# Kernel optimization log

Measured on AMD Instinct MI355X. Metric: run time of the kernel, lower is better.

The kernel has to match this reference:

```python
import jax, jax.numpy as jnp
import numpy as np

# FCHL19 hyperparameters (from init_kwargs defaults)
NSPEC = 4
RCUT = 6.0
NRS2 = 24
NRS3 = 20
ETA2 = 0.32
ETA3 = 2.7
TWO_BODY_DECAY = 1.8
THREE_BODY_WEIGHT = float(np.sqrt(2.7 / np.pi) * 13.4)  # sqrt(eta3/pi)*13.4, as in __init__
THREE_BODY_DECAY = 0.57
PI = float(np.pi)
NPAIRS = NSPEC * (NSPEC + 1) // 2  # 10 unordered element pairs
RS2 = jnp.linspace(0.0, RCUT, NRS2 + 1)[1:]
RS3 = jnp.linspace(0.0, RCUT, NRS3 + 1)[1:]


def setup_inputs() -> dict:
    key = jax.random.key(0)
    k1, k2, k3 = jax.random.split(key, 3)
    B, A = 64, 48
    X = jax.random.uniform(k1, (B, A, 3), jnp.float32, 0.0, 12.0)  # coords in 12 A box
    Z = jax.random.randint(k2, (B, A), 0, NSPEC, dtype=jnp.int32)  # species indices into [1,6,7,8]
    atom_counts = jax.random.randint(k3, (B,), 24, A + 1, dtype=jnp.int32)
    atomIDs = (jnp.arange(B * A, dtype=jnp.int32) % A)
    molIDs = (jnp.arange(B * A, dtype=jnp.int32) // A)
    return {"X": X, "Z": Z, "atomIDs": atomIDs, "molIDs": molIDs, "atom_counts": atom_counts}


def _fchl_rep(X, Z, atom_counts):
    B, A, _ = X.shape
    idx = jnp.arange(A)
    valid = idx[None, :] < atom_counts[:, None]                       # [B,A]
    diff = X[:, :, None, :] - X[:, None, :, :]                        # [B,A,A,3] (X_i - X_j)
    r2 = jnp.sum(diff * diff, axis=-1)
    eye = jnp.eye(A, dtype=bool)
    pmask = valid[:, :, None] & valid[:, None, :] & ~eye              # [B,A,A]
    r = jnp.sqrt(jnp.where(pmask, r2, 1.0))
    within = pmask & (r < RCUT)
    rs = jnp.where(within, r, 1.0)                                    # safe distances
    fc = jnp.where(within, 0.5 * (jnp.cos(PI * rs / RCUT) + 1.0), 0.0)

    # ---- two-body: log-normal radial basis with power-law scaling ----
    s2 = jnp.log1p(ETA2 / (rs * rs))                                  # sigma^2
    mu = jnp.log(rs) - 0.5 * s2
    pref = fc / (rs ** TWO_BODY_DECAY) / (jnp.sqrt(s2) * np.sqrt(2.0 * PI))
    radial2 = (pref[..., None] / RS2) * jnp.exp(
        -(jnp.log(RS2) - mu[..., None]) ** 2 / (2.0 * s2[..., None]))  # [B,A,A,nRs2]
    eoh = jax.nn.one_hot(Z, NSPEC, dtype=X.dtype) * valid[..., None]  # [B,A,S]
    rep2 = jnp.einsum('bijk,bjs->bisk', radial2, eoh).reshape(B, A, NSPEC * NRS2)

    # ---- three-body: ATM-weighted radial x (cos,sin) angular, pairs k>j ----
    rij = rs[:, :, :, None]   # [B,A(i),A(j),1]
    rik = rs[:, :, None, :]   # [B,A(i),1,A(k)]
    rjk = rs[:, None, :, :]   # [B,1,A(j),A(k)]
    cos_i = jnp.einsum('bijx,bikx->bijk', diff, diff) / (rij * rik)
    cos_i = jnp.clip(cos_i, -1.0, 1.0)
    cos_j = (rij * rij + rjk * rjk - rik * rik) / (2.0 * rij * rjk)
    cos_k = (rik * rik + rjk * rjk - rij * rij) / (2.0 * rik * rjk)
    mask3 = (within[:, :, :, None] & within[:, :, None, :]
             & (idx[None, :] > idx[:, None])[None, None, :, :])        # k > j
    ksi3 = THREE_BODY_WEIGHT * (1.0 + 3.0 * cos_i * cos_j * cos_k) \
        / (rij * rik * rjk) ** THREE_BODY_DECAY
    w = jnp.where(mask3, ksi3 * fc[:, :, :, None] * fc[:, :, None, :], 0.0)
    wc = w * cos_i
    ws = w * jnp.sqrt(jnp.clip(1.0 - cos_i * cos_i, 0.0, 1.0))
    d = 0.5 * (rij + rik)                                             # [B,A,A,A]

    # unordered element-pair bin for (Z_j, Z_k)
    ej = Z[:, :, None]
    ek = Z[:, None, :]
    pmin = jnp.minimum(ej, ek)
    pmax = jnp.maximum(ej, ek)
    pidx = pmin * (2 * NSPEC - pmin - 1) // 2 + pmax                  # [B,A,A]
    poh = jax.nn.one_hot(pidx, NPAIRS, dtype=X.dtype)                 # [B,A,A,P]

    def step(carry, Rl):
        rad = jnp.exp(-ETA3 * (d - Rl) ** 2)
        rc = jnp.einsum('bijk,bjkp->bip', wc * rad, poh)
        rsn = jnp.einsum('bijk,bjkp->bip', ws * rad, poh)
        return carry, jnp.stack([rc, rsn], axis=-1)                   # [B,A,P,2]

    _, rep3 = jax.lax.scan(step, 0, RS3)                              # [nRs3,B,A,P,2]
    rep3 = jnp.transpose(rep3, (1, 2, 3, 0, 4)).reshape(B, A, NPAIRS * NRS3 * 2)
    return jnp.concatenate([rep2, rep3], axis=-1)                     # [B,A,496]


def reference(X, Z, atomIDs, molIDs, atom_counts):
    # atomIDs/molIDs are CUDA work-distribution lists; math-irrelevant here.
    return _fchl_rep(X, Z, atom_counts)
```

## Files before the change

kernel.cpp:

```cpp
#include <hip/hip_runtime.h>
#include <math.h>

#define B_MOL 64
#define A_MAX 48
#define NSPEC 4
#define NRS2 24
#define NRS3 20
#define NPAIRS 10
#define REP2 (NSPEC * NRS2)
#define REP3 (NPAIRS * NRS3 * 2)
#define REPTOT (REP2 + REP3)
#define TRIP_CAP 1084

#define RCUT_F 6.0f
#define ETA2_F 0.32f
#define ETA3_F 2.7f
#define PI_F 3.14159265358979323846f
#define W3_F 12.4225780586f
#define SQRT_2PI_F 2.5066282746310002f

__device__ __forceinline__ void decode_tri(int t, int m, int& a_out, int& c_out) {
    const float fm = (float)(2 * m - 1);
    const float disc = fm * fm - 8.0f * (float)t;
    const float sq = __builtin_amdgcn_sqrtf(disc);
    int a = (int)((fm - sq) * 0.5f);
    if (a < 0) a = 0;
    while (a > 0 && (a * (2 * m - 1 - a)) / 2 > t) --a;
    while (((a + 1) * (2 * m - 1 - (a + 1))) / 2 <= t) ++a;
    a_out = a;
    c_out = t - (a * (2 * m - 1 - a)) / 2 + a + 1;
}

__global__ __launch_bounds__(256, 8) void fchl_kernel(
    const float* __restrict__ X, const int* __restrict__ Z,
    const int* __restrict__ atom_counts, float* __restrict__ out)
{
    __shared__ float nb_dx[A_MAX], nb_dy[A_MAX], nb_dz[A_MAX];
    __shared__ float nb_r[A_MAX], nb_r2[A_MAX], nb_rinv[A_MAX];
    __shared__ float nb_fc[A_MAX], nb_mu[A_MAX], nb_i2s2[A_MAX], nb_pref[A_MAX];
    __shared__ int   nb_z[A_MAX], nb_si[A_MAX];
    __shared__ float trip_wc[TRIP_CAP], trip_ws[TRIP_CAP], trip_d[TRIP_CAP];
    __shared__ int   cnt_s[NSPEC];
    __shared__ int   nb_m;

    const int bi = blockIdx.x;
    const int b = bi / A_MAX;
    const int i = bi % A_MAX;
    const int tid = threadIdx.x;
    const int cnt = atom_counts[b];
    float* orow = out + (size_t)bi * REPTOT;

    if (i >= cnt) {
        for (int t = tid; t < REPTOT; t += 256) orow[t] = 0.0f;
        return;
    }

    if (tid < 64) {
        const float xi = X[(b * A_MAX + i) * 3 + 0];
        const float yi = X[(b * A_MAX + i) * 3 + 1];
        const float zi = X[(b * A_MAX + i) * 3 + 2];

        bool flag = false;
        float dx = 0.f, dy = 0.f, dz = 0.f, r = 1.f;
        int zj = 0;
        if (tid < A_MAX && tid < cnt) {
            dx = xi - X[(b * A_MAX + tid) * 3 + 0];
            dy = yi - X[(b * A_MAX + tid) * 3 + 1];
            dz = zi - X[(b * A_MAX + tid) * 3 + 2];
            zj = Z[b * A_MAX + tid];
            r = __builtin_amdgcn_sqrtf(dx * dx + dy * dy + dz * dz);
            flag = (tid != i) && (r < RCUT_F);
        }
        const unsigned long long ms0 = __ballot(flag && zj == 0);
        const unsigned long long ms1 = __ballot(flag && zj == 1);
        const unsigned long long ms2 = __ballot(flag && zj == 2);
        const unsigned long long ms3 = __ballot(flag && zj == 3);
        const unsigned long long mask = ms0 | ms1 | ms2 | ms3;
        if (flag) {
            const unsigned long long below = (1ull << tid) - 1ull;
            const int pos = __popcll(mask & below);
            nb_dx[pos] = dx; nb_dy[pos] = dy; nb_dz[pos] = dz;
            nb_r[pos]  = r;  nb_r2[pos] = r * r;
            nb_rinv[pos] = __builtin_amdgcn_rcpf(r);
            nb_z[pos]  = zj;
            const unsigned long long msp = (zj == 0) ? ms0 : (zj == 1) ? ms1
                                         : (zj == 2) ? ms2 : ms3;
            nb_si[pos] = __popcll(msp & below);
            const float fc = 0.5f * (__cosf(PI_F * r * (1.0f / RCUT_F)) + 1.0f);
            const float lr = __logf(r);
            const float s2 = log1pf(ETA2_F / (r * r));
            nb_fc[pos]   = fc;
            nb_mu[pos]   = lr - 0.5f * s2;
            nb_i2s2[pos] = 0.5f * __builtin_amdgcn_rcpf(s2);
            nb_pref[pos] = fc * __expf(-1.8f * lr) *
                           __builtin_amdgcn_rcpf(__builtin_amdgcn_sqrtf(s2) * SQRT_2PI_F);
        }
        if (tid == 0) {
            cnt_s[0] = (int)__popcll(ms0);
            cnt_s[1] = (int)__popcll(ms1);
            cnt_s[2] = (int)__popcll(ms2);
            cnt_s[3] = (int)__popcll(ms3);
            nb_m = (int)__popcll(mask);
        }
    }
    __syncthreads();

    const int m  = nb_m;
    const int c0 = cnt_s[0], c1 = cnt_s[1], c2 = cnt_s[2], c3 = cnt_s[3];
    const int S0 = (c0 * (c0 - 1)) >> 1;
    const int S1 = c0 * c1, S2 = c0 * c2, S3 = c0 * c3;
    const int S4 = (c1 * (c1 - 1)) >> 1;
    const int S5 = c1 * c2, S6 = c1 * c3;
    const int S7 = (c2 * (c2 - 1)) >> 1;
    const int S8 = c2 * c3;
    const int ntrip = m * (m - 1) / 2;

    for (int t = tid; t < ntrip; t += 256) {
        int a, c;
        decode_tri(t, m, a, c);

        const float rij = nb_r[a], rik = nb_r[c];
        const float r2ij = nb_r2[a], r2ik = nb_r2[c];
        const float rinv_a = nb_rinv[a], rinv_c = nb_rinv[c];
        const float djx = nb_dx[a], djy = nb_dy[a], djz = nb_dz[a];
        const float dkx = nb_dx[c], dky = nb_dy[c], dkz = nb_dz[c];

        float cosi = (djx * dkx + djy * dky + djz * dkz) * rinv_a * rinv_c;
        cosi = fminf(1.0f, fmaxf(-1.0f, cosi));

        const float ex = dkx - djx, ey = dky - djy, ez = dkz - djz;
        const float rjk2 = ex * ex + ey * ey + ez * ez;
        const float rjk = __builtin_amdgcn_sqrtf(rjk2);
        const bool w_jk = (rjk < RCUT_F);
        const float rjke  = w_jk ? rjk : 1.0f;
        const float rjke2 = w_jk ? rjk2 : 1.0f;
        const float rinv_jk = w_jk ? __builtin_amdgcn_rcpf(rjk) : 1.0f;

        const float cosj = (r2ij + rjke2 - r2ik) * 0.5f * rinv_a * rinv_jk;
        const float cosk = (r2ik + rjke2 - r2ij) * 0.5f * rinv_c * rinv_jk;

        const float ksi = W3_F * (1.0f + 3.0f * cosi * cosj * cosk)
                        * __expf(-0.57f * __logf(rij * rik * rjke));
        const float w  = ksi * nb_fc[a] * nb_fc[c];
        const float s1v = fmaxf(1.0f - cosi * cosi, 0.0f);

        const int za = nb_z[a], zc = nb_z[c];
        const int ia = nb_si[a], ic = nb_si[c];
        const int pmn = min(za, zc), pmx = max(za, zc);
        const int p = (pmn * (2 * NSPEC - pmn - 1)) / 2 + pmx;
        int rank;
        if (za == zc) {
            const int cs = (za == 0) ? c0 : (za == 1) ? c1 : (za == 2) ? c2 : c3;
            rank = ia * cs - ((ia * (ia + 1)) >> 1) + (ic - ia - 1);
        } else {
            const int cmx = (pmx == 0) ? c0 : (pmx == 1) ? c1 : (pmx == 2) ? c2 : c3;
            const int iu = (za < zc) ? ia : ic;
            const int iv = (za < zc) ? ic : ia;
            rank = iu * cmx + iv;
        }
        int slot = rank;
        slot += (p > 0) ? S0 : 0;  slot += (p > 1) ? S1 : 0;
        slot += (p > 2) ? S2 : 0;  slot += (p > 3) ? S3 : 0;
        slot += (p > 4) ? S4 : 0;  slot += (p > 5) ? S5 : 0;
        slot += (p > 6) ? S6 : 0;  slot += (p > 7) ? S7 : 0;
        slot += (p > 8) ? S8 : 0;

        trip_wc[slot] = w * cosi;
        trip_ws[slot] = w * __builtin_amdgcn_sqrtf(s1v);
        trip_d[slot]  = 0.5f * (rij + rik);
    }
    __syncthreads();

    if (tid < NPAIRS * NRS3) {
        const int p = tid / NRS3;
        const int l = tid % NRS3;
        const float Rl = 0.3f * (float)(l + 1);
        int s0 = 0;
        s0 += (p > 0) ? S0 : 0;  s0 += (p > 1) ? S1 : 0;
        s0 += (p > 2) ? S2 : 0;  s0 += (p > 3) ? S3 : 0;
        s0 += (p > 4) ? S4 : 0;  s0 += (p > 5) ? S5 : 0;
        s0 += (p > 6) ? S6 : 0;  s0 += (p > 7) ? S7 : 0;
        s0 += (p > 8) ? S8 : 0;
        const int sz = (p == 0) ? S0 : (p == 1) ? S1 : (p == 2) ? S2
                     : (p == 3) ? S3 : (p == 4) ? S4 : (p == 5) ? S5
                     : (p == 6) ? S6 : (p == 7) ? S7 : (p == 8) ? S8
                     : (ntrip - s0);
        const int s1 = s0 + sz;

        float ac0 = 0.0f, as0 = 0.0f, ac1 = 0.0f, as1 = 0.0f;
        int s = s0;
        for (; s + 1 < s1; s += 2) {
            const float d0 = trip_d[s],     d1 = trip_d[s + 1];
            const float dd0 = d0 - Rl,      dd1 = d1 - Rl;
            const float e0 = __expf(-ETA3_F * dd0 * dd0);
            const float e1 = __expf(-ETA3_F * dd1 * dd1);
            ac0 += trip_wc[s] * e0;     as0 += trip_ws[s] * e0;
            ac1 += trip_wc[s + 1] * e1; as1 += trip_ws[s + 1] * e1;
        }
        if (s < s1) {
            const float dd = trip_d[s] - Rl;
            const float e = __expf(-ETA3_F * dd * dd);
            ac0 += trip_wc[s] * e;  as0 += trip_ws[s] * e;
        }
        orow[REP2 + p * (NRS3 * 2) + l * 2 + 0] = ac0 + ac1;
        orow[REP2 + p * (NRS3 * 2) + l * 2 + 1] = as0 + as1;
    } else {
        for (int t2 = tid - 200; t2 < REP2; t2 += 56) {
            const int sp = t2 / NRS2;
            const int n = t2 % NRS2;
            const float Rn = 0.25f * (float)(n + 1);
            const float logRn = __logf(Rn);
            float acc = 0.0f;
            for (int a = 0; a < m; ++a) {
                if (nb_z[a] == sp) {
                    const float dmu = logRn - nb_mu[a];
                    acc += nb_pref[a] * __expf(-dmu * dmu * nb_i2s2[a]);
                }
            }
            orow[t2] = acc * __builtin_amdgcn_rcpf(Rn);
        }
    }
}

extern "C" void kernel_launch(void* const* d_in, const int* in_sizes, int n_in,
                              void* d_out, int out_size, void* d_ws, size_t ws_size,
                              hipStream_t stream) {
    const float* X           = (const float*)d_in[0];
    const int*   Z           = (const int*)d_in[1];
    const int*   atom_counts = (const int*)d_in[4];
    float* out = (float*)d_out;

    fchl_kernel<<<B_MOL * A_MAX, 256, 0, stream>>>(X, Z, atom_counts, out);
}
```

Before: 73.57 us.

## Build neighbor list per wave and overlap two-body with triplet phase

Every wave now builds the neighbor list redundantly, using wave-level ballots and only a wave barrier. This removes the block-wide barrier between neighbor setup and triplet generation. The two-body radial terms move to the last wave and run at the same time as triplet generation on the first three waves. A per-species sorted neighbor index lets the two-body loop skip the species test. Triplet data is packed into one float4 array for single LDS loads. The trade-offs are redundant work across waves and benign same-value LDS write races, and triplet generation now uses 192 threads instead of 256.

```diff
diff --git a/kernel.cpp b/kernel.cpp
--- a/kernel.cpp
+++ b/kernel.cpp
@@ -38,15 +38,14 @@
     __shared__ float nb_dx[A_MAX], nb_dy[A_MAX], nb_dz[A_MAX];
     __shared__ float nb_r[A_MAX], nb_r2[A_MAX], nb_rinv[A_MAX];
     __shared__ float nb_fc[A_MAX], nb_mu[A_MAX], nb_i2s2[A_MAX], nb_pref[A_MAX];
-    __shared__ int   nb_z[A_MAX], nb_si[A_MAX];
-    __shared__ float trip_wc[TRIP_CAP], trip_ws[TRIP_CAP], trip_d[TRIP_CAP];
-    __shared__ int   cnt_s[NSPEC];
-    __shared__ int   nb_m;
+    __shared__ int   nb_z[A_MAX], nb_si[A_MAX], snb[A_MAX];
+    __shared__ float4 trip4[TRIP_CAP];
 
     const int bi = blockIdx.x;
     const int b = bi / A_MAX;
     const int i = bi % A_MAX;
     const int tid = threadIdx.x;
+    const int lane = tid & 63;
     const int cnt = atom_counts[b];
     float* orow = out + (size_t)bi * REPTOT;
 
@@ -55,58 +54,55 @@
         return;
     }
 
-    if (tid < 64) {
-        const float xi = X[(b * A_MAX + i) * 3 + 0];
-        const float yi = X[(b * A_MAX + i) * 3 + 1];
-        const float zi = X[(b * A_MAX + i) * 3 + 2];
-
-        bool flag = false;
-        float dx = 0.f, dy = 0.f, dz = 0.f, r = 1.f;
-        int zj = 0;
-        if (tid < A_MAX && tid < cnt) {
-            dx = xi - X[(b * A_MAX + tid) * 3 + 0];
-            dy = yi - X[(b * A_MAX + tid) * 3 + 1];
-            dz = zi - X[(b * A_MAX + tid) * 3 + 2];
-            zj = Z[b * A_MAX + tid];
-            r = __builtin_amdgcn_sqrtf(dx * dx + dy * dy + dz * dz);
-            flag = (tid != i) && (r < RCUT_F);
-        }
-        const unsigned long long ms0 = __ballot(flag && zj == 0);
-        const unsigned long long ms1 = __ballot(flag && zj == 1);
-        const unsigned long long ms2 = __ballot(flag && zj == 2);
-        const unsigned long long ms3 = __ballot(flag && zj == 3);
-        const unsigned long long mask = ms0 | ms1 | ms2 | ms3;
-        if (flag) {
-            const unsigned long long below = (1ull << tid) - 1ull;
-            const int pos = __popcll(mask & below);
-            nb_dx[pos] = dx; nb_dy[pos] = dy; nb_dz[pos] = dz;
-            nb_r[pos]  = r;  nb_r2[pos] = r * r;
-            nb_rinv[pos] = __builtin_amdgcn_rcpf(r);
-            nb_z[pos]  = zj;
-            const unsigned long long msp = (zj == 0) ? ms0 : (zj == 1) ? ms1
-                                         : (zj == 2) ? ms2 : ms3;
-            nb_si[pos] = __popcll(msp & below);
-            const float fc = 0.5f * (__cosf(PI_F * r * (1.0f / RCUT_F)) + 1.0f);
-            const float lr = __logf(r);
-            const float s2 = log1pf(ETA2_F / (r * r));
-            nb_fc[pos]   = fc;
-            nb_mu[pos]   = lr - 0.5f * s2;
-            nb_i2s2[pos] = 0.5f * __builtin_amdgcn_rcpf(s2);
-            nb_pref[pos] = fc * __expf(-1.8f * lr) *
-                           __builtin_amdgcn_rcpf(__builtin_amdgcn_sqrtf(s2) * SQRT_2PI_F);
-        }
-        if (tid == 0) {
-            cnt_s[0] = (int)__popcll(ms0);
-            cnt_s[1] = (int)__popcll(ms1);
-            cnt_s[2] = (int)__popcll(ms2);
-            cnt_s[3] = (int)__popcll(ms3);
-            nb_m = (int)__popcll(mask);
-        }
-    }
-    __syncthreads();
-
-    const int m  = nb_m;
-    const int c0 = cnt_s[0], c1 = cnt_s[1], c2 = cnt_s[2], c3 = cnt_s[3];
+    const float xi = X[(b * A_MAX + i) * 3 + 0];
+    const float yi = X[(b * A_MAX + i) * 3 + 1];
+    const float zi = X[(b * A_MAX + i) * 3 + 2];
+
+    bool flag = false;
+    float dx = 0.f, dy = 0.f, dz = 0.f, r = 1.f;
+    int zj = 0;
+    if (lane < A_MAX && lane < cnt) {
+        dx = xi - X[(b * A_MAX + lane) * 3 + 0];
+        dy = yi - X[(b * A_MAX + lane) * 3 + 1];
+        dz = zi - X[(b * A_MAX + lane) * 3 + 2];
+        zj = Z[b * A_MAX + lane];
+        r = __builtin_amdgcn_sqrtf(dx * dx + dy * dy + dz * dz);
+        flag = (lane != i) && (r < RCUT_F);
+    }
+    const unsigned long long ms0 = __ballot(flag && zj == 0);
+    const unsigned long long ms1 = __ballot(flag && zj == 1);
+    const unsigned long long ms2 = __ballot(flag && zj == 2);
+    const unsigned long long ms3 = __ballot(flag && zj == 3);
+    const unsigned long long mask = ms0 | ms1 | ms2 | ms3;
+    const int m  = (int)__popcll(mask);
+    const int c0 = (int)__popcll(ms0), c1 = (int)__popcll(ms1);
+    const int c2 = (int)__popcll(ms2), c3 = (int)__popcll(ms3);
+
+    if (flag) {
+        const unsigned long long below = (1ull << lane) - 1ull;
+        const int pos = __popcll(mask & below);
+        nb_dx[pos] = dx; nb_dy[pos] = dy; nb_dz[pos] = dz;
+        nb_r[pos]  = r;  nb_r2[pos] = r * r;
+        nb_rinv[pos] = __builtin_amdgcn_rcpf(r);
+        nb_z[pos]  = zj;
+        const unsigned long long msp = (zj == 0) ? ms0 : (zj == 1) ? ms1
+                                     : (zj == 2) ? ms2 : ms3;
+        const int si = __popcll(msp & below);
+        nb_si[pos] = si;
+        const int ss = (zj == 0) ? 0 : (zj == 1) ? c0
+                     : (zj == 2) ? (c0 + c1) : (c0 + c1 + c2);
+        snb[ss + si] = pos;
+        const float fc = 0.5f * (__cosf(PI_F * r * (1.0f / RCUT_F)) + 1.0f);
+        const float lr = __logf(r);
+        const float s2 = log1pf(ETA2_F / (r * r));
+        nb_fc[pos]   = fc;
+        nb_mu[pos]   = lr - 0.5f * s2;
+        nb_i2s2[pos] = 0.5f * __builtin_amdgcn_rcpf(s2);
+        nb_pref[pos] = fc * __expf(-1.8f * lr) *
+                       __builtin_amdgcn_rcpf(__builtin_amdgcn_sqrtf(s2) * SQRT_2PI_F);
+    }
+    __builtin_amdgcn_wave_barrier();
+
     const int S0 = (c0 * (c0 - 1)) >> 1;
     const int S1 = c0 * c1, S2 = c0 * c2, S3 = c0 * c3;
     const int S4 = (c1 * (c1 - 1)) >> 1;
@@ -115,59 +111,79 @@
     const int S8 = c2 * c3;
     const int ntrip = m * (m - 1) / 2;
 
-    for (int t = tid; t < ntrip; t += 256) {
-        int a, c;
-        decode_tri(t, m, a, c);
-
-        const float rij = nb_r[a], rik = nb_r[c];
-        const float r2ij = nb_r2[a], r2ik = nb_r2[c];
-        const float rinv_a = nb_rinv[a], rinv_c = nb_rinv[c];
-        const float djx = nb_dx[a], djy = nb_dy[a], djz = nb_dz[a];
-        const float dkx = nb_dx[c], dky = nb_dy[c], dkz = nb_dz[c];
-
-        float cosi = (djx * dkx + djy * dky + djz * dkz) * rinv_a * rinv_c;
-        cosi = fminf(1.0f, fmaxf(-1.0f, cosi));
-
-        const float ex = dkx - djx, ey = dky - djy, ez = dkz - djz;
-        const float rjk2 = ex * ex + ey * ey + ez * ez;
-        const float rjk = __builtin_amdgcn_sqrtf(rjk2);
-        const bool w_jk = (rjk < RCUT_F);
-        const float rjke  = w_jk ? rjk : 1.0f;
-        const float rjke2 = w_jk ? rjk2 : 1.0f;
-        const float rinv_jk = w_jk ? __builtin_amdgcn_rcpf(rjk) : 1.0f;
-
-        const float cosj = (r2ij + rjke2 - r2ik) * 0.5f * rinv_a * rinv_jk;
-        const float cosk = (r2ik + rjke2 - r2ij) * 0.5f * rinv_c * rinv_jk;
-
-        const float ksi = W3_F * (1.0f + 3.0f * cosi * cosj * cosk)
-                        * __expf(-0.57f * __logf(rij * rik * rjke));
-        const float w  = ksi * nb_fc[a] * nb_fc[c];
-        const float s1v = fmaxf(1.0f - cosi * cosi, 0.0f);
-
-        const int za = nb_z[a], zc = nb_z[c];
-        const int ia = nb_si[a], ic = nb_si[c];
-        const int pmn = min(za, zc), pmx = max(za, zc);
-        const int p = (pmn * (2 * NSPEC - pmn - 1)) / 2 + pmx;
-        int rank;
-        if (za == zc) {
-            const int cs = (za == 0) ? c0 : (za == 1) ? c1 : (za == 2) ? c2 : c3;
-            rank = ia * cs - ((ia * (ia + 1)) >> 1) + (ic - ia - 1);
-        } else {
-            const int cmx = (pmx == 0) ? c0 : (pmx == 1) ? c1 : (pmx == 2) ? c2 : c3;
-            const int iu = (za < zc) ? ia : ic;
-            const int iv = (za < zc) ? ic : ia;
-            rank = iu * cmx + iv;
-        }
-        int slot = rank;
-        slot += (p > 0) ? S0 : 0;  slot += (p > 1) ? S1 : 0;
-        slot += (p > 2) ? S2 : 0;  slot += (p > 3) ? S3 : 0;
-        slot += (p > 4) ? S4 : 0;  slot += (p > 5) ? S5 : 0;
-        slot += (p > 6) ? S6 : 0;  slot += (p > 7) ? S7 : 0;
-        slot += (p > 8) ? S8 : 0;
-
-        trip_wc[slot] = w * cosi;
-        trip_ws[slot] = w * __builtin_amdgcn_sqrtf(s1v);
-        trip_d[slot]  = 0.5f * (rij + rik);
+    if (tid >= 192) {
+        for (int t2 = lane; t2 < REP2; t2 += 64) {
+            const int sp = t2 / NRS2;
+            const int n  = t2 % NRS2;
+            const float Rn = 0.25f * (float)(n + 1);
+            const float logRn = __logf(Rn);
+            const int ss = (sp == 0) ? 0 : (sp == 1) ? c0
+                         : (sp == 2) ? (c0 + c1) : (c0 + c1 + c2);
+            const int ce = ss + ((sp == 0) ? c0 : (sp == 1) ? c1
+                               : (sp == 2) ? c2 : c3);
+            float acc = 0.0f;
+            for (int a2 = ss; a2 < ce; ++a2) {
+                const int idx = snb[a2];
+                const float dmu = logRn - nb_mu[idx];
+                acc += nb_pref[idx] * __expf(-dmu * dmu * nb_i2s2[idx]);
+            }
+            orow[t2] = acc * __builtin_amdgcn_rcpf(Rn);
+        }
+    } else {
+        for (int t = tid; t < ntrip; t += 192) {
+            int a, c;
+            decode_tri(t, m, a, c);
+
+            const float rij = nb_r[a], rik = nb_r[c];
+            const float r2ij = nb_r2[a], r2ik = nb_r2[c];
+            const float rinv_a = nb_rinv[a], rinv_c = nb_rinv[c];
+            const float djx = nb_dx[a], djy = nb_dy[a], djz = nb_dz[a];
+            const float dkx = nb_dx[c], dky = nb_dy[c], dkz = nb_dz[c];
+
+            float cosi = (djx * dkx + djy * dky + djz * dkz) * rinv_a * rinv_c;
+            cosi = fminf(1.0f, fmaxf(-1.0f, cosi));
+
+            const float ex = dkx - djx, ey = dky - djy, ez = dkz - djz;
+            const float rjk2 = ex * ex + ey * ey + ez * ez;
+            const float rjk = __builtin_amdgcn_sqrtf(rjk2);
+            const bool w_jk = (rjk < RCUT_F);
+            const float rjke  = w_jk ? rjk : 1.0f;
+            const float rjke2 = w_jk ? rjk2 : 1.0f;
+            const float rinv_jk = w_jk ? __builtin_amdgcn_rcpf(rjk) : 1.0f;
+
+            const float cosj = (r2ij + rjke2 - r2ik) * 0.5f * rinv_a * rinv_jk;
+            const float cosk = (r2ik + rjke2 - r2ij) * 0.5f * rinv_c * rinv_jk;
+
+            const float ksi = W3_F * (1.0f + 3.0f * cosi * cosj * cosk)
+                            * __expf(-0.57f * __logf(rij * rik * rjke));
+            const float w  = ksi * nb_fc[a] * nb_fc[c];
+            const float s1v = fmaxf(1.0f - cosi * cosi, 0.0f);
+
+            const int za = nb_z[a], zc = nb_z[c];
+            const int ia = nb_si[a], ic = nb_si[c];
+            const int pmn = min(za, zc), pmx = max(za, zc);
+            const int p = (pmn * (2 * NSPEC - pmn - 1)) / 2 + pmx;
+            int rank;
+            if (za == zc) {
+                const int cs = (za == 0) ? c0 : (za == 1) ? c1 : (za == 2) ? c2 : c3;
+                rank = ia * cs - ((ia * (ia + 1)) >> 1) + (ic - ia - 1);
+            } else {
+                const int cmx = (pmx == 0) ? c0 : (pmx == 1) ? c1 : (pmx == 2) ? c2 : c3;
+                const int iu = (za < zc) ? ia : ic;
+                const int iv = (za < zc) ? ic : ia;
+                rank = iu * cmx + iv;
+            }
+            int slot = rank;
+            slot += (p > 0) ? S0 : 0;  slot += (p > 1) ? S1 : 0;
+            slot += (p > 2) ? S2 : 0;  slot += (p > 3) ? S3 : 0;
+            slot += (p > 4) ? S4 : 0;  slot += (p > 5) ? S5 : 0;
+            slot += (p > 6) ? S6 : 0;  slot += (p > 7) ? S7 : 0;
+            slot += (p > 8) ? S8 : 0;
+
+            trip4[slot] = make_float4(w * cosi,
+                                      w * __builtin_amdgcn_sqrtf(s1v),
+                                      0.5f * (rij + rik), 0.0f);
+        }
     }
     __syncthreads();
 
@@ -190,35 +206,22 @@
         float ac0 = 0.0f, as0 = 0.0f, ac1 = 0.0f, as1 = 0.0f;
         int s = s0;
         for (; s + 1 < s1; s += 2) {
-            const float d0 = trip_d[s],     d1 = trip_d[s + 1];
-            const float dd0 = d0 - Rl,      dd1 = d1 - Rl;
+            const float4 t0 = trip4[s];
+            const float4 t1 = trip4[s + 1];
+            const float dd0 = t0.z - Rl, dd1 = t1.z - Rl;
             const float e0 = __expf(-ETA3_F * dd0 * dd0);
             const float e1 = __expf(-ETA3_F * dd1 * dd1);
-            ac0 += trip_wc[s] * e0;     as0 += trip_ws[s] * e0;
-            ac1 += trip_wc[s + 1] * e1; as1 += trip_ws[s + 1] * e1;
+            ac0 += t0.x * e0;  as0 += t0.y * e0;
+            ac1 += t1.x * e1;  as1 += t1.y * e1;
         }
         if (s < s1) {
-            const float dd = trip_d[s] - Rl;
+            const float4 t0 = trip4[s];
+            const float dd = t0.z - Rl;
             const float e = __expf(-ETA3_F * dd * dd);
-            ac0 += trip_wc[s] * e;  as0 += trip_ws[s] * e;
+            ac0 += t0.x * e;  as0 += t0.y * e;
         }
         orow[REP2 + p * (NRS3 * 2) + l * 2 + 0] = ac0 + ac1;
         orow[REP2 + p * (NRS3 * 2) + l * 2 + 1] = as0 + as1;
-    } else {
-        for (int t2 = tid - 200; t2 < REP2; t2 += 56) {
-            const int sp = t2 / NRS2;
-            const int n = t2 % NRS2;
-            const float Rn = 0.25f * (float)(n + 1);
-            const float logRn = __logf(Rn);
-            float acc = 0.0f;
-            for (int a = 0; a < m; ++a) {
-                if (nb_z[a] == sp) {
-                    const float dmu = logRn - nb_mu[a];
-                    acc += nb_pref[a] * __expf(-dmu * dmu * nb_i2s2[a]);
-                }
-            }
-            orow[t2] = acc * __builtin_amdgcn_rcpf(Rn);
-        }
     }
 }
 
```

After: 72.23 us. About the same (-1.8%).
